# Performance work log

Measured on AMD Instinct MI355X. Metric: run time of the kernel, lower is better.

Reference implementation:

```python
import jax, jax.numpy as jnp
import numpy as np

N_LAYER = 4
N_HEAD = 8
N_EMBD = 512
HEAD_SIZE = N_EMBD // N_HEAD
VOCAB = 32000
BLOCK = 2048
WINDOW = 64
N_GLOBAL = 16
N_RANDOM = 16
B = 2
T = 2048


def setup_inputs() -> dict:
    key = jax.random.key(0)
    ks = jax.random.split(key, 24)
    s = 0.02
    inp = {
        "tok_emb": jax.random.normal(ks[0], (VOCAB, N_EMBD), jnp.float32) * s,
        "pos_emb": jax.random.normal(ks[1], (BLOCK, N_EMBD), jnp.float32) * s,
        "Wq": jax.random.normal(ks[2], (N_LAYER, N_HEAD, N_EMBD, HEAD_SIZE), jnp.float32) * s,
        "Wk": jax.random.normal(ks[3], (N_LAYER, N_HEAD, N_EMBD, HEAD_SIZE), jnp.float32) * s,
        "Wv": jax.random.normal(ks[4], (N_LAYER, N_HEAD, N_EMBD, HEAD_SIZE), jnp.float32) * s,
        "Wproj": jax.random.normal(ks[5], (N_LAYER, N_EMBD, N_EMBD), jnp.float32) * s,
        "bproj": jnp.zeros((N_LAYER, N_EMBD), jnp.float32),
        "ln1_g": jnp.ones((N_LAYER, N_EMBD), jnp.float32),
        "ln1_b": jnp.zeros((N_LAYER, N_EMBD), jnp.float32),
        "ln2_g": jnp.ones((N_LAYER, N_EMBD), jnp.float32),
        "ln2_b": jnp.zeros((N_LAYER, N_EMBD), jnp.float32),
        "W1": jax.random.normal(ks[6], (N_LAYER, N_EMBD, 4 * N_EMBD), jnp.float32) * s,
        "b1": jnp.zeros((N_LAYER, 4 * N_EMBD), jnp.float32),
        "W2": jax.random.normal(ks[7], (N_LAYER, 4 * N_EMBD, N_EMBD), jnp.float32) * s,
        "b2": jnp.zeros((N_LAYER, N_EMBD), jnp.float32),
        "lnf_g": jnp.ones((N_EMBD,), jnp.float32),
        "lnf_b": jnp.zeros((N_EMBD,), jnp.float32),
        "Wout": jax.random.normal(ks[8], (N_EMBD, VOCAB), jnp.float32) * s,
        "bout": jnp.zeros((VOCAB,), jnp.float32),
        "input_tokens": jax.random.randint(ks[9], (B, T), 0, VOCAB, jnp.int32),
        "random_cols": jax.random.randint(ks[10], (N_LAYER, N_HEAD, T, N_RANDOM), 0, T, jnp.int32),
    }
    return inp


def _layernorm(x, g, b):
    mu = jnp.mean(x, axis=-1, keepdims=True)
    var = jnp.var(x, axis=-1, keepdims=True)
    return (x - mu) * jax.lax.rsqrt(var + 1e-5) * g + b


def _static_masks(t):
    rows = jnp.arange(t)[:, None]
    cols = jnp.arange(t)[None, :]
    causal = rows >= cols
    local = (cols >= rows - WINDOW + 1) & (cols <= rows)
    glob = (rows < N_GLOBAL) | (cols < N_GLOBAL)
    return local | glob, causal  # base [T,T], causal [T,T]


def _random_mask(rc):  # rc: [H, T, R] -> [H, T, T] bool
    h, t, r = rc.shape
    m = jnp.zeros((h, t, t), dtype=bool)
    hi = jnp.arange(h)[:, None, None]
    ri = jnp.arange(t)[None, :, None]
    return m.at[hi, ri, rc].set(True)


def _forward(tok_emb, pos_emb, Wq, Wk, Wv, Wproj, bproj, ln1_g, ln1_b, ln2_g, ln2_b,
             W1, b1, W2, b2, lnf_g, lnf_b, Wout, bout, input_tokens, random_cols):
    b, t = input_tokens.shape
    x = tok_emb[input_tokens] + pos_emb[:t]  # [B,T,C]
    base, causal = _static_masks(t)
    scale = HEAD_SIZE ** -0.5
    neg_inf = jnp.finfo(x.dtype).min
    for l in range(N_LAYER):
        xn = _layernorm(x, ln1_g[l], ln1_b[l])
        q = jnp.einsum('btc,hcd->bhtd', xn, Wq[l])
        k = jnp.einsum('btc,hcd->bhtd', xn, Wk[l])
        v = jnp.einsum('btc,hcd->bhtd', xn, Wv[l])
        w = jnp.einsum('bhtd,bhsd->bhts', q, k) * scale  # [B,H,T,T]
        final = (base[None] | _random_mask(random_cols[l])) & causal[None]  # [H,T,T]
        w = jnp.where(final[None], w, neg_inf)
        w = jax.nn.softmax(w, axis=-1)
        attn = jnp.einsum('bhts,bhsd->bhtd', w, v)  # [B,H,T,hs]
        attn = attn.transpose(0, 2, 1, 3).reshape(b, t, N_EMBD)
        x = x + attn @ Wproj[l] + bproj[l]
        xn = _layernorm(x, ln2_g[l], ln2_b[l])
        h = jax.nn.relu(xn @ W1[l] + b1[l])
        x = x + h @ W2[l] + b2[l]
    x = _layernorm(x, lnf_g, lnf_b)
    return x @ Wout + bout  # logits [B,T,V]


def reference(tok_emb, pos_emb, Wq, Wk, Wv, Wproj, bproj, ln1_g, ln1_b, ln2_g, ln2_b,
              W1, b1, W2, b2, lnf_g, lnf_b, Wout, bout, input_tokens, random_cols):
    return _forward(tok_emb, pos_emb, Wq, Wk, Wv, Wproj, bproj, ln1_g, ln1_b, ln2_g, ln2_b,
                    W1, b1, W2, b2, lnf_g, lnf_b, Wout, bout, input_tokens, random_cols)
```

## Files before the change

### kernel.cpp

```cpp
#include <hip/hip_runtime.h>
#include <hip/hip_bf16.h>

#define NLAYER 4
#define NHEAD 8
#define CEMB 512
#define HS 64
#define VOCAB_N 32000
#define SEQT 2048
#define BATCH_N 2
#define MROWS (BATCH_N * SEQT)
#define WIN 64
#define NGLOB 16
#define NRAND 16
#define QB 16

typedef __attribute__((ext_vector_type(8))) __bf16 bf16x8;
typedef __attribute__((ext_vector_type(4))) float f32x4;
typedef __attribute__((ext_vector_type(8))) unsigned short u16x8;

__device__ __forceinline__ unsigned short f2bf(float f) {
    unsigned u = __float_as_uint(f);
    u += 0x7fffu + ((u >> 16) & 1u);
    return (unsigned short)(u >> 16);
}
__device__ __forceinline__ float bf2f(unsigned short v) {
    return __uint_as_float((unsigned)v << 16);
}

__device__ __forceinline__ void stage16(const unsigned short* g, unsigned short* l) {
    __builtin_amdgcn_global_load_lds(
        (const __attribute__((address_space(1))) void*)g,
        (__attribute__((address_space(3))) void*)l, 16, 0, 0);
}

__global__ __launch_bounds__(256) void transpose_all_kernel(
    const float* __restrict__ Wq, const float* __restrict__ Wk,
    const float* __restrict__ Wv, const float* __restrict__ Wproj,
    const float* __restrict__ W1, const float* __restrict__ W2,
    const float* __restrict__ Wout,
    unsigned short* __restrict__ wqkvT, unsigned short* __restrict__ wprojT,
    unsigned short* __restrict__ w1T, unsigned short* __restrict__ w2T,
    unsigned short* __restrict__ woutT)
{
    __shared__ float tle[64][65];
    const int bid = blockIdx.x;
    const float* src; unsigned short* dst; int Ks, Ns, k0, n0;
    if (bid < 768) {
        const int tile = bid & 7, rest = bid >> 3;
        const int l = rest / 24, r2 = rest % 24;
        const int sel = r2 >> 3, h = r2 & 7;
        const float* W = (sel == 0) ? Wq : (sel == 1) ? Wk : Wv;
        src = W + (size_t)(l * 8 + h) * 512 * 64;
        dst = wqkvT + ((size_t)l * 1536 + sel * 512 + h * 64) * 512;
        Ks = 512; Ns = 64; k0 = tile * 64; n0 = 0;
    } else if (bid < 1024) {
        const int idx = bid - 768, l = idx >> 6, t6 = idx & 63;
        src = Wproj + (size_t)l * 512 * 512;
        dst = wprojT + (size_t)l * 512 * 512;
        Ks = 512; Ns = 512; k0 = (t6 >> 3) * 64; n0 = (t6 & 7) * 64;
    } else if (bid < 2048) {
        const int idx = bid - 1024, l = idx >> 8, t8 = idx & 255;
        src = W1 + (size_t)l * 512 * 2048;
        dst = w1T + (size_t)l * 2048 * 512;
        Ks = 512; Ns = 2048; k0 = (t8 >> 5) * 64; n0 = (t8 & 31) * 64;
    } else if (bid < 3072) {
        const int idx = bid - 2048, l = idx >> 8, t8 = idx & 255;
        src = W2 + (size_t)l * 2048 * 512;
        dst = w2T + (size_t)l * 512 * 2048;
        Ks = 2048; Ns = 512; k0 = (t8 >> 3) * 64; n0 = (t8 & 7) * 64;
    } else {
        const int idx = bid - 3072;
        src = Wout; dst = woutT;
        Ks = 512; Ns = 32000; k0 = (idx / 500) * 64; n0 = (idx % 500) * 64;
    }
    const int tid = threadIdx.x;
    #pragma unroll
    for (int i = 0; i < 16; ++i) {
        const int idx = tid + i * 256;
        const int r = idx >> 6, c = idx & 63;
        tle[r][c] = src[(size_t)(k0 + r) * Ns + n0 + c];
    }
    __syncthreads();
    #pragma unroll
    for (int i = 0; i < 16; ++i) {
        const int idx = tid + i * 256;
        const int c = idx >> 6, r = idx & 63;
        dst[(size_t)(n0 + c) * Ks + k0 + r] = f2bf(tle[r][c]);
    }
}

__global__ __launch_bounds__(256) void embed_kernel(
    const float* __restrict__ tok_emb, const float* __restrict__ pos_emb,
    const int* __restrict__ toks, float* __restrict__ x)
{
    int i = blockIdx.x * 256 + threadIdx.x;
    int m = i >> 7;
    int c = (i & 127) << 2;
    int tok = toks[m];
    const float4 a = *(const float4*)&tok_emb[(size_t)tok * CEMB + c];
    const float4 p = *(const float4*)&pos_emb[(size_t)(m & (SEQT - 1)) * CEMB + c];
    float4 o;
    o.x = a.x + p.x; o.y = a.y + p.y; o.z = a.z + p.z; o.w = a.w + p.w;
    *(float4*)&x[(size_t)m * CEMB + c] = o;
}

__global__ __launch_bounds__(256) void ln_kernel(
    const float* __restrict__ x, const float* __restrict__ g,
    const float* __restrict__ b, unsigned short* __restrict__ out)
{
    const int wave = threadIdx.x >> 6, lane = threadIdx.x & 63;
    const int m = blockIdx.x * 4 + wave;
    const float* row = x + (size_t)m * CEMB;
    const float4 v0 = *(const float4*)&row[lane * 8];
    const float4 v1 = *(const float4*)&row[lane * 8 + 4];
    float s  = v0.x + v0.y + v0.z + v0.w + v1.x + v1.y + v1.z + v1.w;
    float s2 = v0.x*v0.x + v0.y*v0.y + v0.z*v0.z + v0.w*v0.w
             + v1.x*v1.x + v1.y*v1.y + v1.z*v1.z + v1.w*v1.w;
    #pragma unroll
    for (int off = 32; off > 0; off >>= 1) {
        s  += __shfl_xor(s, off);
        s2 += __shfl_xor(s2, off);
    }
    const float mu  = s * (1.f / CEMB);
    const float var = s2 * (1.f / CEMB) - mu * mu;
    const float rs  = rsqrtf(var + 1e-5f);
    const float vals[8] = {v0.x, v0.y, v0.z, v0.w, v1.x, v1.y, v1.z, v1.w};
    u16x8 o;
    #pragma unroll
    for (int j = 0; j < 8; ++j)
        o[j] = f2bf((vals[j] - mu) * rs * g[lane * 8 + j] + b[lane * 8 + j]);
    *(u16x8*)&out[(size_t)m * CEMB + lane * 8] = o;
}

template<int MODE, int NF>
__global__ __launch_bounds__(256) void gemm_kernel(
    const unsigned short* __restrict__ A, const unsigned short* __restrict__ Bt,
    const float* __restrict__ bias, const float* resid, void* outp,
    int M, int N, int K)
{
    __shared__ unsigned short sa[3][128 * 32];
    __shared__ unsigned short sb[3][NF * 32 * 32];
    const int tid = threadIdx.x;
    const int lane = tid & 63;
    const int wave = tid >> 6;
    const int wr = wave >> 1, wc = wave & 1;
    const int m0 = blockIdx.y * 128;
    const int n0 = blockIdx.x * (NF * 32);

    const int c0a = (wave * 2) * 64 + lane;
    const int c1a = (wave * 2 + 1) * 64 + lane;
    const int r0 = c0a >> 2, kk0 = (((c0a & 3) ^ ((r0 >> 1) & 3)) * 8);
    const int r1 = c1a >> 2, kk1 = (((c1a & 3) ^ ((r1 >> 1) & 3)) * 8);
    const unsigned short* ga0 = A + (size_t)(m0 + r0) * K + kk0;
    const unsigned short* ga1 = A + (size_t)(m0 + r1) * K + kk1;
    const int o0 = (wave * 2) * 512;
    const int o1 = (wave * 2 + 1) * 512;
    const int cb0 = (NF == 4) ? c0a : wave * 64 + lane;
    const int cb1 = c1a;
    const int rb0 = cb0 >> 2, kb0 = (((cb0 & 3) ^ ((rb0 >> 1) & 3)) * 8);
    const int rb1 = cb1 >> 2, kb1 = (((cb1 & 3) ^ ((rb1 >> 1) & 3)) * 8);
    const unsigned short* gb0 = Bt + (size_t)(n0 + rb0) * K + kb0;
    const unsigned short* gb1 = Bt + (size_t)(n0 + rb1) * K + kb1;
    const int ob0 = (NF == 4) ? o0 : wave * 512;
    const int ob1 = o1;

    f32x4 acc[4][NF] = {};
    const int lq = lane >> 4;
    const int fr = lane & 15;

    auto STAGE = [&](int tile, int buf) {
        const int kk = tile << 5;
        stage16(ga0 + kk, &sa[buf][o0]);
        stage16(ga1 + kk, &sa[buf][o1]);
        stage16(gb0 + kk, &sb[buf][ob0]);
        if constexpr (NF == 4) stage16(gb1 + kk, &sb[buf][ob1]);
    };

    const int nt = K >> 5;
    STAGE(0, 0);
    STAGE(1, 1);

    int cur = 0;
    for (int t = 0; t < nt; ++t) {
        if (t + 1 < nt) {
            if constexpr (NF == 2) asm volatile("s_waitcnt vmcnt(3)" ::: "memory");
            else                   asm volatile("s_waitcnt vmcnt(4)" ::: "memory");
        } else {
            asm volatile("s_waitcnt vmcnt(0)" ::: "memory");
        }
        __builtin_amdgcn_s_barrier();
        __builtin_amdgcn_sched_barrier(0);

        if (t + 2 < nt) {
            int b2 = cur + 2; if (b2 >= 3) b2 -= 3;
            STAGE(t + 2, b2);
        }

        bf16x8 af[4], bfr[NF];
        #pragma unroll
        for (int i = 0; i < 4; ++i) {
            const int Ra = wr * 64 + i * 16 + fr;
            af[i] = *reinterpret_cast<const bf16x8*>(
                &sa[cur][Ra * 32 + (((lq ^ ((Ra >> 1) & 3))) << 3)]);
        }
        #pragma unroll
        for (int i = 0; i < NF; ++i) {
            const int Rb = wc * (NF * 16) + i * 16 + fr;
            bfr[i] = *reinterpret_cast<const bf16x8*>(
                &sb[cur][Rb * 32 + (((lq ^ ((Rb >> 1) & 3))) << 3)]);
        }
        #pragma unroll
        for (int mi = 0; mi < 4; ++mi)
            #pragma unroll
            for (int ni = 0; ni < NF; ++ni)
                acc[mi][ni] = __builtin_amdgcn_mfma_f32_16x16x32_bf16(af[mi], bfr[ni], acc[mi][ni], 0, 0, 0);

        cur = (cur == 2) ? 0 : cur + 1;
    }

    #pragma unroll
    for (int mi = 0; mi < 4; ++mi) {
        #pragma unroll
        for (int ni = 0; ni < NF; ++ni) {
            const int gc = n0 + wc * (NF * 16) + ni * 16 + fr;
            const float bv = (MODE != 0) ? bias[gc] : 0.f;
            #pragma unroll
            for (int r = 0; r < 4; ++r) {
                const int gr = m0 + wr * 64 + mi * 16 + lq * 4 + r;
                float v = acc[mi][ni][r] + bv;
                if (MODE == 1) v += resid[(size_t)gr * N + gc];
                if (MODE == 2) v = fmaxf(v, 0.f);
                if (MODE == 0 || MODE == 2) {
                    ((unsigned short*)outp)[(size_t)gr * N + gc] = f2bf(v);
                } else {
                    ((float*)outp)[(size_t)gr * N + gc] = v;
                }
            }
        }
    }
}

__global__ __launch_bounds__(512) void gemm_logits_kernel(
    const unsigned short* __restrict__ A, const unsigned short* __restrict__ Bt,
    const float* __restrict__ bias, float* __restrict__ outp,
    int M, int N, int K)
{
    __shared__ unsigned short sa[2][256 * 32];
    __shared__ unsigned short sb[2][128 * 32];
    const int tid = threadIdx.x;
    const int lane = tid & 63;
    const int wave = tid >> 6;
    const int wr = wave >> 1, wc = wave & 1;

    const int flat = blockIdx.y * gridDim.x + blockIdx.x;
    const int q = (gridDim.x * gridDim.y) >> 3;
    const int nl = (flat & 7) * q + (flat >> 3);
    const int by = nl & 15;
    const int bx = nl >> 4;
    const int m0 = by * 256;
    const int n0 = bx * 128;

    const int c0a = (wave * 2) * 64 + lane;
    const int c1a = (wave * 2 + 1) * 64 + lane;
    const int r0 = c0a >> 2, kk0 = (((c0a & 3) ^ ((r0 >> 1) & 3)) * 8);
    const int r1 = c1a >> 2, kk1 = (((c1a & 3) ^ ((r1 >> 1) & 3)) * 8);
    const unsigned short* ga0 = A + (size_t)(m0 + r0) * K + kk0;
    const unsigned short* ga1 = A + (size_t)(m0 + r1) * K + kk1;
    const int o0 = (wave * 2) * 512;
    const int o1 = (wave * 2 + 1) * 512;
    const int cb0 = wave * 64 + lane;
    const int rb0 = cb0 >> 2, kb0 = (((cb0 & 3) ^ ((rb0 >> 1) & 3)) * 8);
    const unsigned short* gb0 = Bt + (size_t)(n0 + rb0) * K + kb0;
    const int ob0 = wave * 512;

    f32x4 acc[4][4] = {};
    const int lq = lane >> 4;
    const int fr = lane & 15;

    auto STAGE = [&](int t, int buf) {
        const int kk = t << 5;
        stage16(ga0 + kk, &sa[buf][o0]);
        stage16(ga1 + kk, &sa[buf][o1]);
        stage16(gb0 + kk, &sb[buf][ob0]);
    };

    const int nt = K >> 5;
    STAGE(0, 0);
    __syncthreads();
    int cur = 0;
    for (int t = 0; t < nt; ++t) {
        if (t + 1 < nt) STAGE(t + 1, cur ^ 1);
        bf16x8 af[4], bfr[4];
        #pragma unroll
        for (int i = 0; i < 4; ++i) {
            const int Ra = wr * 64 + i * 16 + fr;
            af[i] = *reinterpret_cast<const bf16x8*>(
                &sa[cur][Ra * 32 + (((lq ^ ((Ra >> 1) & 3))) << 3)]);
        }
        #pragma unroll
        for (int i = 0; i < 4; ++i) {
            const int Rb = wc * 64 + i * 16 + fr;
            bfr[i] = *reinterpret_cast<const bf16x8*>(
                &sb[cur][Rb * 32 + (((lq ^ ((Rb >> 1) & 3))) << 3)]);
        }
        #pragma unroll
        for (int mi = 0; mi < 4; ++mi)
            #pragma unroll
            for (int ni = 0; ni < 4; ++ni)
                acc[mi][ni] = __builtin_amdgcn_mfma_f32_16x16x32_bf16(af[mi], bfr[ni], acc[mi][ni], 0, 0, 0);
        __syncthreads();
        cur ^= 1;
    }

    #pragma unroll
    for (int mi = 0; mi < 4; ++mi) {
        #pragma unroll
        for (int ni = 0; ni < 4; ++ni) {
            const int gc = n0 + wc * 64 + ni * 16 + fr;
            const float bv = bias[gc];
            #pragma unroll
            for (int r = 0; r < 4; ++r) {
                const int gr = m0 + wr * 64 + mi * 16 + lq * 4 + r;
                outp[(size_t)gr * N + gc] = acc[mi][ni][r] + bv;
            }
        }
    }
}

__global__ __launch_bounds__(256) void attn_kernel(
    const unsigned short* __restrict__ qkv, const int* __restrict__ rc,
    unsigned short* __restrict__ attnout)
{
    __shared__ unsigned short Kw[80 * 64];
    __shared__ unsigned short Vw[80 * 64];
    __shared__ float ewA[4][64];
    __shared__ float cwW[4][40];
    __shared__ int   cwC[4][40];

    const int tid = threadIdx.x;
    const int wave = tid >> 6, lane = tid & 63;
    const int bid = blockIdx.x;
    const int tb = bid & 127;
    const int h = (bid >> 7) & 7;
    const int b = bid >> 10;
    const int t0 = tb * QB;
    const int base = t0 - 63;

    const unsigned short* kb = qkv + (size_t)b * SEQT * 1536 + 512 + h * 64;
    const unsigned short* vb = qkv + (size_t)b * SEQT * 1536 + 1024 + h * 64;

    for (int c = tid; c < 79 * 8; c += 256) {
        const int r = c >> 3, j = c & 7;
        const int col = base + r;
        u16x8 kv = {0, 0, 0, 0, 0, 0, 0, 0};
        u16x8 vv = {0, 0, 0, 0, 0, 0, 0, 0};
        if (col >= 0) {
            kv = *(const u16x8*)&kb[(size_t)col * 1536 + j * 8];
            vv = *(const u16x8*)&vb[(size_t)col * 1536 + j * 8];
        }
        *(u16x8*)&Kw[r * 64 + ((j ^ (r & 7)) * 8)] = kv;
        *(u16x8*)&Vw[r * 64 + j * 8] = vv;
    }
    __syncthreads();

    for (int u = 0; u < 4; ++u) {
        const int Q = wave * 4 + u;
        const int t = t0 + Q;
        const int m = b * SEQT + t;

        u16x8 qreg[8];
        #pragma unroll
        for (int j = 0; j < 8; ++j)
            qreg[j] = *(const u16x8*)&qkv[(size_t)m * 1536 + h * 64 + j * 8];

        const int row = Q + lane;
        const int colA = base + row;
        float sA;
        {
            float s = 0.f;
            #pragma unroll
            for (int j = 0; j < 8; ++j) {
                const u16x8 kc = *(const u16x8*)&Kw[row * 64 + ((j ^ (row & 7)) * 8)];
                #pragma unroll
                for (int e = 0; e < 8; ++e)
                    s += bf2f(kc[e]) * bf2f(qreg[j][e]);
            }
            sA = (colA >= NGLOB) ? s * 0.125f : -1e30f;
        }

        int colB = 0;
        bool vB = false;
        if (lane < NGLOB) {
            colB = lane;
            vB = (lane <= t);
        } else if (lane < 32) {
            colB = rc[((size_t)h * SEQT + t) * NRAND + (lane - 16)];
            vB = (colB >= NGLOB) && (colB <= t - WIN);
        }
        #pragma unroll
        for (int j = 0; j < 15; ++j) {
            const int cj = __shfl(colB, 16 + j);
            if (lane >= 16 && lane < 32 && (lane - 16) > j && cj == colB) vB = false;
        }

        float sB = -1e30f;
        if (vB) {
            float s = 0.f;
            const unsigned short* kr = &kb[(size_t)colB * 1536];
            #pragma unroll
            for (int j = 0; j < 8; ++j) {
                const u16x8 kc = *(const u16x8*)&kr[j * 8];
                #pragma unroll
                for (int e = 0; e < 8; ++e)
                    s += bf2f(kc[e]) * bf2f(qreg[j][e]);
            }
            sB = s * 0.125f;
        }

        float mx = fmaxf(sA, sB);
        #pragma unroll
        for (int off = 32; off > 0; off >>= 1) mx = fmaxf(mx, __shfl_xor(mx, off));
        const float e0 = (colA >= NGLOB) ? __expf(sA - mx) : 0.f;
        const float e1 = vB ? __expf(sB - mx) : 0.f;
        float sum = e0 + e1;
        #pragma unroll
        for (int off = 32; off > 0; off >>= 1) sum += __shfl_xor(sum, off);
        const float inv = 1.f / sum;

        ewA[wave][lane] = e0;
        const unsigned long long bm = __ballot(vB);
        const int nB = __popcll(bm);
        const int pos = __popcll(bm & ((1ull << lane) - 1ull));
        if (vB) { cwC[wave][pos] = colB; cwW[wave][pos] = e1; }
        if (lane >= 32 && lane < 36) {
            const int p = nB + (lane - 32);
            cwC[wave][p] = 0; cwW[wave][p] = 0.f;
        }

        float acc = 0.f;
        #pragma unroll 8
        for (int s = 0; s < 64; ++s)
            acc += ewA[wave][s] * bf2f(Vw[(Q + s) * 64 + lane]);

        const int nB4 = (nB + 3) & ~3;
        for (int i = 0; i < nB4; i += 4) {
            const float w0 = cwW[wave][i + 0], w1 = cwW[wave][i + 1];
            const float w2 = cwW[wave][i + 2], w3 = cwW[wave][i + 3];
            const int   c0 = cwC[wave][i + 0], c1 = cwC[wave][i + 1];
            const int   c2 = cwC[wave][i + 2], c3 = cwC[wave][i + 3];
            const float x0 = bf2f(vb[(size_t)c0 * 1536 + lane]);
            const float x1 = bf2f(vb[(size_t)c1 * 1536 + lane]);
            const float x2 = bf2f(vb[(size_t)c2 * 1536 + lane]);
            const float x3 = bf2f(vb[(size_t)c3 * 1536 + lane]);
            acc += w0 * x0 + w1 * x1 + w2 * x2 + w3 * x3;
        }

        attnout[(size_t)m * CEMB + h * 64 + lane] = f2bf(acc * inv);
    }
}

extern "C" void kernel_launch(void* const* d_in, const int* in_sizes, int n_in,
                              void* d_out, int out_size, void* d_ws, size_t ws_size,
                              hipStream_t stream)
{
    const float* tok_emb = (const float*)d_in[0];
    const float* pos_emb = (const float*)d_in[1];
    const float* Wq    = (const float*)d_in[2];
    const float* Wk    = (const float*)d_in[3];
    const float* Wv    = (const float*)d_in[4];
    const float* Wproj = (const float*)d_in[5];
    const float* bproj = (const float*)d_in[6];
    const float* ln1g  = (const float*)d_in[7];
    const float* ln1b  = (const float*)d_in[8];
    const float* ln2g  = (const float*)d_in[9];
    const float* ln2b  = (const float*)d_in[10];
    const float* W1    = (const float*)d_in[11];
    const float* b1    = (const float*)d_in[12];
    const float* W2    = (const float*)d_in[13];
    const float* b2    = (const float*)d_in[14];
    const float* lnfg  = (const float*)d_in[15];
    const float* lnfb  = (const float*)d_in[16];
    const float* Wout  = (const float*)d_in[17];
    const float* bout  = (const float*)d_in[18];
    const int*   toks  = (const int*)d_in[19];
    const int*   rcols = (const int*)d_in[20];
    (void)in_sizes; (void)n_in; (void)out_size; (void)ws_size;

    char* ws = (char*)d_ws;
    size_t off = 0;
    auto ALLOC = [&](size_t bytes) -> void* {
        void* p = ws + off;
        off += (bytes + 255) & ~(size_t)255;
        return p;
    };
    float*          x      = (float*)ALLOC((size_t)MROWS * CEMB * 4);
    unsigned short* xnbf   = (unsigned short*)ALLOC((size_t)MROWS * CEMB * 2);
    unsigned short* qkv    = (unsigned short*)ALLOC((size_t)MROWS * 1536 * 2);
    unsigned short* attnbf = (unsigned short*)ALLOC((size_t)MROWS * CEMB * 2);
    unsigned short* hbf    = (unsigned short*)ALLOC((size_t)MROWS * 2048 * 2);
    unsigned short* wqkvT  = (unsigned short*)ALLOC((size_t)NLAYER * 1536 * 512 * 2);
    unsigned short* wprojT = (unsigned short*)ALLOC((size_t)NLAYER * 512 * 512 * 2);
    unsigned short* w1T    = (unsigned short*)ALLOC((size_t)NLAYER * 2048 * 512 * 2);
    unsigned short* w2T    = (unsigned short*)ALLOC((size_t)NLAYER * 512 * 2048 * 2);
    unsigned short* woutT  = (unsigned short*)ALLOC((size_t)VOCAB_N * 512 * 2);

    transpose_all_kernel<<<7072, 256, 0, stream>>>(
        Wq, Wk, Wv, Wproj, W1, W2, Wout, wqkvT, wprojT, w1T, w2T, woutT);

    embed_kernel<<<2048, 256, 0, stream>>>(tok_emb, pos_emb, toks, x);

    for (int l = 0; l < NLAYER; ++l) {
        ln_kernel<<<1024, 256, 0, stream>>>(x, ln1g + l * CEMB, ln1b + l * CEMB, xnbf);
        gemm_kernel<0, 2><<<dim3(24, 32), 256, 0, stream>>>(
            xnbf, wqkvT + (size_t)l * 1536 * 512, nullptr, nullptr, qkv, MROWS, 1536, 512);
        attn_kernel<<<2048, 256, 0, stream>>>(qkv, rcols + (size_t)l * NHEAD * SEQT * NRAND, attnbf);
        gemm_kernel<1, 2><<<dim3(8, 32), 256, 0, stream>>>(
            attnbf, wprojT + (size_t)l * 512 * 512, bproj + l * CEMB, x, x, MROWS, 512, 512);
        ln_kernel<<<1024, 256, 0, stream>>>(x, ln2g + l * CEMB, ln2b + l * CEMB, xnbf);
        gemm_kernel<2, 4><<<dim3(16, 32), 256, 0, stream>>>(
            xnbf, w1T + (size_t)l * 2048 * 512, b1 + l * 2048, nullptr, hbf, MROWS, 2048, 512);
        gemm_kernel<1, 2><<<dim3(8, 32), 256, 0, stream>>>(
            hbf, w2T + (size_t)l * 512 * 2048, b2 + l * CEMB, x, x, MROWS, 512, 2048);
    }
    ln_kernel<<<1024, 256, 0, stream>>>(x, lnfg, lnfb, xnbf);
    gemm_logits_kernel<<<dim3(250, 16), 512, 0, stream>>>(
        xnbf, woutT, bout, (float*)d_out, MROWS, VOCAB_N, 512);
}
```

Before: 1.021 ms.

## Compute windowed attention P·V with MFMA over a transposed V tile

The per-query scalar loop over the 64-wide local window becomes a 16x16x32 bf16 MFMA. Softmax weights are staged as bf16 in a shared P tile and V is stored transposed in shared memory, so a block's 16 queries are multiplied against the window tile in one pass. The random/global columns remain a scalar gather loop, now done per output column after a block barrier. This adds a transposed LDS store, an extra sync, and rounds the probabilities to bf16, which reduces precision. Only the attention kernel changes, and it is a small part of the whole forward pass.

Result: no change. 1.013 ms (median of 2 runs) (-0.9%).

```diff
diff --git a/kernel.cpp b/kernel.cpp
--- a/kernel.cpp
+++ b/kernel.cpp
@@ -13,6 +13,8 @@
 #define NGLOB 16
 #define NRAND 16
 #define QB 16
+#define VTW 104
+#define PSW 104
 
 typedef __attribute__((ext_vector_type(8))) __bf16 bf16x8;
 typedef __attribute__((ext_vector_type(4))) float f32x4;
@@ -332,13 +334,16 @@
     unsigned short* __restrict__ attnout)
 {
     __shared__ unsigned short Kw[80 * 64];
-    __shared__ unsigned short Vw[80 * 64];
-    __shared__ float ewA[4][64];
-    __shared__ float cwW[4][40];
-    __shared__ int   cwC[4][40];
+    __shared__ unsigned short Vt[64 * VTW];
+    __shared__ unsigned short Ps[16 * PSW];
+    __shared__ float rWs[16][40];
+    __shared__ short rCs[16][40];
+    __shared__ int   nBs[16];
+    __shared__ float qinv[16];
 
     const int tid = threadIdx.x;
     const int wave = tid >> 6, lane = tid & 63;
+    const int lq = lane >> 4, fr = lane & 15;
     const int bid = blockIdx.x;
     const int tb = bid & 127;
     const int h = (bid >> 7) & 7;
@@ -359,7 +364,13 @@
             vv = *(const u16x8*)&vb[(size_t)col * 1536 + j * 8];
         }
         *(u16x8*)&Kw[r * 64 + ((j ^ (r & 7)) * 8)] = kv;
-        *(u16x8*)&Vw[r * 64 + j * 8] = vv;
+        #pragma unroll
+        for (int e = 0; e < 8; ++e)
+            Vt[(j * 8 + e) * VTW + r] = vv[e];
+    }
+    for (int i = tid; i < 64 * 17; i += 256) {
+        const int d = i / 17, s = 79 + (i - d * 17);
+        Vt[d * VTW + s] = 0;
     }
     __syncthreads();
 
@@ -425,37 +436,48 @@
         float sum = e0 + e1;
         #pragma unroll
         for (int off = 32; off > 0; off >>= 1) sum += __shfl_xor(sum, off);
-        const float inv = 1.f / sum;
-
-        ewA[wave][lane] = e0;
+
+        Ps[Q * PSW + Q + lane] = f2bf(e0);
+        if (lane < 32) Ps[Q * PSW + ((Q + 64 + lane) % 96)] = 0;
+
         const unsigned long long bm = __ballot(vB);
         const int nB = __popcll(bm);
         const int pos = __popcll(bm & ((1ull << lane) - 1ull));
-        if (vB) { cwC[wave][pos] = colB; cwW[wave][pos] = e1; }
+        if (vB) { rCs[Q][pos] = (short)colB; rWs[Q][pos] = e1; }
         if (lane >= 32 && lane < 36) {
             const int p = nB + (lane - 32);
-            cwC[wave][p] = 0; cwW[wave][p] = 0.f;
-        }
-
-        float acc = 0.f;
-        #pragma unroll 8
-        for (int s = 0; s < 64; ++s)
-            acc += ewA[wave][s] * bf2f(Vw[(Q + s) * 64 + lane]);
-
-        const int nB4 = (nB + 3) & ~3;
-        for (int i = 0; i < nB4; i += 4) {
-            const float w0 = cwW[wave][i + 0], w1 = cwW[wave][i + 1];
-            const float w2 = cwW[wave][i + 2], w3 = cwW[wave][i + 3];
-            const int   c0 = cwC[wave][i + 0], c1 = cwC[wave][i + 1];
-            const int   c2 = cwC[wave][i + 2], c3 = cwC[wave][i + 3];
-            const float x0 = bf2f(vb[(size_t)c0 * 1536 + lane]);
-            const float x1 = bf2f(vb[(size_t)c1 * 1536 + lane]);
-            const float x2 = bf2f(vb[(size_t)c2 * 1536 + lane]);
-            const float x3 = bf2f(vb[(size_t)c3 * 1536 + lane]);
-            acc += w0 * x0 + w1 * x1 + w2 * x2 + w3 * x3;
-        }
-
-        attnout[(size_t)m * CEMB + h * 64 + lane] = f2bf(acc * inv);
+            rCs[Q][p] = 0; rWs[Q][p] = 0.f;
+        }
+        if (lane == 0) { nBs[Q] = nB; qinv[Q] = 1.f / sum; }
+    }
+    __syncthreads();
+
+    const int dmine = wave * 16 + fr;
+    f32x4 of = {0.f, 0.f, 0.f, 0.f};
+    #pragma unroll
+    for (int ks = 0; ks < 3; ++ks) {
+        const int s0 = ks * 32 + lq * 8;
+        const bf16x8 ap = *reinterpret_cast<const bf16x8*>(&Ps[fr * PSW + s0]);
+        const bf16x8 bv = *reinterpret_cast<const bf16x8*>(&Vt[dmine * VTW + s0]);
+        of = __builtin_amdgcn_mfma_f32_16x16x32_bf16(ap, bv, of, 0, 0, 0);
+    }
+
+    #pragma unroll
+    for (int r = 0; r < 4; ++r) {
+        const int q2 = lq * 4 + r;
+        float acc = of[r];
+        const int nb4 = (nBs[q2] + 3) & ~3;
+        for (int i = 0; i < nb4; i += 4) {
+            const float w0 = rWs[q2][i + 0], w1 = rWs[q2][i + 1];
+            const float w2 = rWs[q2][i + 2], w3 = rWs[q2][i + 3];
+            const int   c0 = rCs[q2][i + 0], c1 = rCs[q2][i + 1];
+            const int   c2 = rCs[q2][i + 2], c3 = rCs[q2][i + 3];
+            acc += w0 * bf2f(vb[(size_t)c0 * 1536 + dmine])
+                 + w1 * bf2f(vb[(size_t)c1 * 1536 + dmine])
+                 + w2 * bf2f(vb[(size_t)c2 * 1536 + dmine])
+                 + w3 * bf2f(vb[(size_t)c3 * 1536 + dmine]);
+        }
+        attnout[(size_t)(b * SEQT + t0 + q2) * CEMB + h * 64 + dmine] = f2bf(acc * qinv[q2]);
     }
 }
 
```
